# Kernel optimization log

Hardware: AMD Instinct MI355X
Metric: run time of the kernel (lower is better)

## Reference

```python
import jax, jax.numpy as jnp
import numpy as np

N = 262144      # total nodes
G = 256         # graphs
P = 1024        # nodes per graph (k=None sort pool keeps all)
E = 4194304     # edges
F_IN = 128
H = 32
C = 10          # out capsules / classes
OUT_LEN = 16
IN_LEN = 96     # 3 * 32 concat
NUM_ITERS = 3


def setup_inputs() -> dict:
    key = jax.random.key(0)
    ks = jax.random.split(key, 12)
    x = jax.random.normal(ks[0], (N, F_IN), jnp.float32)
    # edges within each graph of size P
    src = jax.random.randint(ks[1], (E,), 0, N)
    off = jax.random.randint(ks[2], (E,), 0, P)
    dst = (src // P) * P + off
    edge_index = jnp.stack([src, dst]).astype(jnp.int64)
    batch = jnp.repeat(jnp.arange(G), P).astype(jnp.int64)
    W1 = jax.random.normal(ks[3], (F_IN, H), jnp.float32) / np.sqrt(F_IN)
    b1 = jnp.zeros((H,), jnp.float32)
    W2 = jax.random.normal(ks[4], (H, H), jnp.float32) / np.sqrt(H)
    b2 = jnp.zeros((H,), jnp.float32)
    W3 = jax.random.normal(ks[5], (H, H), jnp.float32) / np.sqrt(H)
    b3 = jnp.zeros((H,), jnp.float32)
    caps_W = jax.random.normal(ks[6], (C, OUT_LEN, IN_LEN), jnp.float32) * 0.05
    return {"x": x, "edge_index": edge_index, "batch": batch,
            "W1": W1, "b1": b1, "W2": W2, "b2": b2, "W3": W3, "b3": b3,
            "caps_W": caps_W}


def _position_encoding(length, dim):
    pos = jnp.arange(length, dtype=jnp.float32)[:, None]
    i = jnp.arange(dim // 2, dtype=jnp.float32)[None, :]
    ang = pos / jnp.power(10000.0, 2.0 * i / dim)
    return jnp.stack([jnp.sin(ang), jnp.cos(ang)], axis=-1).reshape(length, dim)


def _squash(v, eps=1e-12):
    n2 = jnp.sum(v * v, axis=-1, keepdims=True)
    return (n2 / (1.0 + n2)) * v / jnp.sqrt(n2 + eps)


def reference(x, edge_index, batch, W1, b1, W2, b2, W3, b3, caps_W):
    src, dst = edge_index[0], edge_index[1]
    # remove_self_loops, then GCNConv re-adds self loops with weight 1
    mask = (src != dst).astype(x.dtype)
    deg = jax.ops.segment_sum(mask, dst, num_segments=N) + 1.0
    dis = jax.lax.rsqrt(deg)                         # deg^{-1/2}
    enorm = dis[src] * dis[dst] * mask               # [E]

    def gcn(h, W, b):
        h = h @ W                                    # [N,H]
        agg = jax.ops.segment_sum(h[src] * enorm[:, None], dst, num_segments=N)
        agg = agg + h * (dis * dis)[:, None]         # self-loop term deg^{-1}
        return jnp.tanh(agg + b)

    x1 = gcn(x, W1, b1)
    x2 = gcn(x1, W2, b2)
    x3 = gcn(x2, W3, b3)
    h = jnp.concatenate([x1, x2, x3], axis=-1)       # [N, 96]

    # global_sort_pool (k=None): per-graph sort by last channel, descending
    hg = h.reshape(G, P, IN_LEN)
    order = jnp.argsort(-hg[:, :, -1], axis=1)
    hs = jnp.take_along_axis(hg, order[:, :, None], axis=1)  # [G,P,96]
    hs = hs + _position_encoding(P, IN_LEN)[None]

    # CapsuleLinear, shared weight: priors [G, C, P, OUT_LEN]
    priors = jnp.einsum('oji,gki->gokj', caps_W, hs)

    # k-means routing
    v = jnp.mean(priors, axis=2, keepdims=True)      # [G,C,1,OUT_LEN]
    for _ in range(NUM_ITERS):
        vn = v / (jnp.linalg.norm(v, axis=-1, keepdims=True) + 1e-12)
        logits = jnp.sum(priors * vn, axis=-1, keepdims=True)  # [G,C,P,1]
        prob = jax.nn.softmax(logits, axis=2)
        v = jnp.sum(prob * priors, axis=2, keepdims=True)
    out = _squash(v)[:, :, 0, :]                     # [G, C, OUT_LEN]
    return jnp.linalg.norm(out, axis=-1)             # [G, C]
```

## Files before the change

kernel.cpp:

```cpp
#include <hip/hip_runtime.h>
#include <hip/hip_fp16.h>
#include <cstdint>
#include <cstddef>

#define N_NODES   262144
#define NG        256
#define PP        1024
#define NE        4194304
#define FIN       128
#define HH        32
#define NC        10
#define OL        16
#define IL        96
#define NITER     3
#define ECHUNK    4096
#define NCHUNK    (NE/ECHUNK)
#define ECAP      18432
#define HSTR      36

typedef _Float16 half8 __attribute__((ext_vector_type(8)));
typedef float f32x4 __attribute__((ext_vector_type(4)));

__global__ void k_hist(const int* __restrict__ ei, unsigned* __restrict__ histT) {
  __shared__ unsigned lh[NG];
  int t = threadIdx.x, b = blockIdx.x;
  lh[t] = 0;
  __syncthreads();
  int base = b * ECHUNK;
  for (int q = t; q < ECHUNK; q += 256) {
    int e = base + q;
    int s = ei[e], d = ei[NE + e];
    if (s != d) atomicAdd(&lh[s >> 10], 1u);
  }
  __syncthreads();
  histT[t * NCHUNK + b] = lh[t];
}

__global__ void k_scanA(const unsigned* __restrict__ histT, unsigned* __restrict__ cbaseT,
                        unsigned* __restrict__ gtot) {
  __shared__ unsigned wtot[4];
  int t = threadIdx.x, g = blockIdx.x;
  int lane = t & 63, wv = t >> 6;
  uint4 hv = *(const uint4*)(histT + (size_t)g * NCHUNK + t * 4);
  unsigned s0 = hv.x, s1 = s0 + hv.y, s2 = s1 + hv.z, s3 = s2 + hv.w;
  unsigned tsum = s3, sc = tsum;
  for (int d = 1; d < 64; d <<= 1) {
    unsigned v = __shfl_up(sc, d, 64);
    if (lane >= d) sc += v;
  }
  if (lane == 63) wtot[wv] = sc;
  __syncthreads();
  unsigned woff = 0;
  for (int w = 0; w < wv; ++w) woff += wtot[w];
  unsigned base = woff + sc - tsum;
  cbaseT[(size_t)(t * 4 + 0) * NG + g] = base;
  cbaseT[(size_t)(t * 4 + 1) * NG + g] = base + s0;
  cbaseT[(size_t)(t * 4 + 2) * NG + g] = base + s1;
  cbaseT[(size_t)(t * 4 + 3) * NG + g] = base + s2;
  if (t == 255) gtot[g] = woff + sc;
}

__global__ void k_scanB(const unsigned* __restrict__ gtot, unsigned* __restrict__ gbase) {
  __shared__ unsigned wtot[4];
  int t = threadIdx.x;
  int lane = t & 63, wv = t >> 6;
  unsigned x = gtot[t], sc = x;
  for (int d = 1; d < 64; d <<= 1) {
    unsigned v = __shfl_up(sc, d, 64);
    if (lane >= d) sc += v;
  }
  if (lane == 63) wtot[wv] = sc;
  __syncthreads();
  unsigned woff = 0;
  for (int w = 0; w < wv; ++w) woff += wtot[w];
  gbase[t] = woff + sc - x;
  if (t == 255) gbase[256] = woff + sc;
}

__global__ void k_scatter(const int* __restrict__ ei, const unsigned* __restrict__ cbaseT,
                          const unsigned* __restrict__ gbase, unsigned* __restrict__ epack) {
  __shared__ unsigned lcur[NG];
  int t = threadIdx.x, b = blockIdx.x;
  lcur[t] = gbase[t] + cbaseT[(size_t)b * NG + t];
  __syncthreads();
  int base = b * ECHUNK;
  for (int q = t; q < ECHUNK; q += 256) {
    int e = base + q;
    int s = ei[e], d = ei[NE + e];
    if (s != d) {
      int g = s >> 10;
      unsigned pos = atomicAdd(&lcur[g], 1u);
      epack[pos] = (unsigned)(s & 1023) | ((unsigned)(d & 1023) << 10);
    }
  }
}

__global__ __launch_bounds__(256) void k_dstsort(const unsigned* __restrict__ epack,
                          const unsigned* __restrict__ gbase,
                          unsigned short* __restrict__ esrc16,
                          unsigned* __restrict__ dstptr) {
  __shared__ unsigned shist[PP];
  __shared__ unsigned wsum[256];
  __shared__ unsigned cur[PP];
  int t = threadIdx.x, g = blockIdx.x;
  unsigned e0 = gbase[g], e1 = gbase[g + 1];
  for (int i = t; i < PP; i += 256) shist[i] = 0;
  __syncthreads();
  for (unsigned e = e0 + t; e < e1; e += 256)
    atomicAdd(&shist[(epack[e] >> 10) & 1023], 1u);
  __syncthreads();
  unsigned h0 = shist[4 * t], h1 = shist[4 * t + 1], h2 = shist[4 * t + 2], h3 = shist[4 * t + 3];
  unsigned tsum = h0 + h1 + h2 + h3;
  wsum[t] = tsum;
  __syncthreads();
  for (int off = 1; off < 256; off <<= 1) {
    unsigned v = (t >= off) ? wsum[t - off] : 0u;
    __syncthreads();
    wsum[t] += v;
    __syncthreads();
  }
  unsigned excl = wsum[t] - tsum;
  unsigned c0 = excl, c1 = c0 + h0, c2 = c1 + h1, c3 = c2 + h2;
  cur[4 * t] = c0; cur[4 * t + 1] = c1; cur[4 * t + 2] = c2; cur[4 * t + 3] = c3;
  unsigned* dp = dstptr + (size_t)g * (PP + 1);
  dp[4 * t] = c0; dp[4 * t + 1] = c1; dp[4 * t + 2] = c2; dp[4 * t + 3] = c3;
  if (t == 0) dp[PP] = e1 - e0;
  __syncthreads();
  unsigned short* eg = esrc16 + (size_t)g * ECAP;
  for (unsigned e = e0 + t; e < e1; e += 256) {
    unsigned pk = epack[e];
    unsigned so = pk & 1023, dofs = (pk >> 10) & 1023;
    unsigned pos = atomicAdd(&cur[dofs], 1u);
    if (pos < ECAP) eg[pos] = (unsigned short)so;
  }
}

__global__ void k_dis(const unsigned* __restrict__ dstptr, float* __restrict__ dis) {
  int n = blockIdx.x * 256 + threadIdx.x;
  int g = n >> 10, k = n & 1023;
  const unsigned* dp = dstptr + (size_t)g * (PP + 1) + k;
  float deg = (float)(dp[1] - dp[0]);
  dis[n] = 1.0f / sqrtf(deg + 1.0f);
}

__device__ __forceinline__ void gcn_layer(float* hsl, const float* dg, const unsigned* dp,
                                          const unsigned short* eg, const float* bias,
                                          int coloff, const float* Wn, float* hbase, int t) {
  float4 bl[8];
#pragma unroll
  for (int j = 0; j < 8; ++j) bl[j] = ((const float4*)bias)[j];
  if (Wn) {
#pragma unroll
    for (int pp = 0; pp < 8; ++pp) {
      int p = t + pp * 512;
      hsl[(p >> 2) * HSTR + 32 + (p & 3)] = Wn[p];
    }
  }
  float xn[2][32];
#pragma unroll
  for (int pth = 0; pth < 2; ++pth) {
    int k = t + pth * 512;
    float dk = dg[k];
    unsigned e0 = dp[k], e1 = dp[k + 1];
    if (e1 > (unsigned)ECAP) e1 = ECAP;
    float4 acc[8];
    const float* sp = &hsl[k * HSTR];
#pragma unroll
    for (int j = 0; j < 8; ++j) acc[j] = *(const float4*)(sp + 4 * j);
    unsigned e = e0;
    for (; e + 1 < e1; e += 2) {
      int s0 = eg[e], s1 = eg[e + 1];
      const float* q0 = &hsl[s0 * HSTR];
      const float* q1 = &hsl[s1 * HSTR];
#pragma unroll
      for (int j = 0; j < 8; ++j) {
        float4 a = *(const float4*)(q0 + 4 * j);
        float4 b2 = *(const float4*)(q1 + 4 * j);
        acc[j].x += a.x + b2.x; acc[j].y += a.y + b2.y;
        acc[j].z += a.z + b2.z; acc[j].w += a.w + b2.w;
      }
    }
    if (e < e1) {
      int s0 = eg[e];
      const float* q0 = &hsl[s0 * HSTR];
#pragma unroll
      for (int j = 0; j < 8; ++j) {
        float4 a = *(const float4*)(q0 + 4 * j);
        acc[j].x += a.x; acc[j].y += a.y; acc[j].z += a.z; acc[j].w += a.w;
      }
    }
#pragma unroll
    for (int j = 0; j < 8; ++j) {
      xn[pth][4 * j + 0] = tanhf(dk * acc[j].x + bl[j].x);
      xn[pth][4 * j + 1] = tanhf(dk * acc[j].y + bl[j].y);
      xn[pth][4 * j + 2] = tanhf(dk * acc[j].z + bl[j].z);
      xn[pth][4 * j + 3] = tanhf(dk * acc[j].w + bl[j].w);
    }
    float* hr = hbase + (size_t)k * IL + coloff;
#pragma unroll
    for (int j = 0; j < 8; ++j) {
      float4 s;
      s.x = xn[pth][4 * j]; s.y = xn[pth][4 * j + 1];
      s.z = xn[pth][4 * j + 2]; s.w = xn[pth][4 * j + 3];
      *(float4*)(hr + 4 * j) = s;
    }
  }
  __syncthreads();
  if (Wn) {
#pragma unroll
    for (int pth = 0; pth < 2; ++pth) {
      int k = t + pth * 512;
      float dk = dg[k];
      float4 o4[8];
#pragma unroll
      for (int j = 0; j < 8; ++j) { o4[j].x = 0.f; o4[j].y = 0.f; o4[j].z = 0.f; o4[j].w = 0.f; }
#pragma unroll
      for (int c = 0; c < 32; ++c) {
        float xc = xn[pth][c];
#pragma unroll
        for (int j4 = 0; j4 < 8; ++j4) {
          float4 w = *(const float4*)&hsl[(c * 8 + j4) * HSTR + 32];
          o4[j4].x += xc * w.x; o4[j4].y += xc * w.y;
          o4[j4].z += xc * w.z; o4[j4].w += xc * w.w;
        }
      }
      float* op = &hsl[k * HSTR];
#pragma unroll
      for (int j4 = 0; j4 < 8; ++j4) {
        float4 s;
        s.x = o4[j4].x * dk; s.y = o4[j4].y * dk;
        s.z = o4[j4].z * dk; s.w = o4[j4].w * dk;
        *(float4*)(op + 4 * j4) = s;
      }
    }
    __syncthreads();
  }
}

__global__ __launch_bounds__(512) void k_gcn(const float* __restrict__ x,
                                             const float* __restrict__ dis,
                                             const unsigned short* __restrict__ esrc16,
                                             const unsigned* __restrict__ dstptr,
                                             const float* __restrict__ W1, const float* __restrict__ b1,
                                             const float* __restrict__ W2, const float* __restrict__ b2,
                                             const float* __restrict__ W3, const float* __restrict__ b3,
                                             float* __restrict__ h) {
  __shared__ float hsl[PP * HSTR];
  int t = threadIdx.x, g = blockIdx.x;
  const float* dg = dis + (size_t)g * PP;
  const unsigned* dp = dstptr + (size_t)g * (PP + 1);
  const unsigned short* eg = esrc16 + (size_t)g * ECAP;
  float* hbase = h + (size_t)g * PP * IL;

#pragma unroll
  for (int pp = 0; pp < 8; ++pp) {
    int p = t + pp * 512;
    hsl[(p >> 2) * HSTR + 32 + (p & 3)] = W1[p];
  }
  __syncthreads();

  {
    int cg = t & 3, ng = t >> 2;
    int row0 = ng * 8;
    const float* xr = x + ((size_t)g * PP + row0) * FIN;
    float acc[8][8];
#pragma unroll
    for (int r = 0; r < 8; ++r)
#pragma unroll
      for (int j = 0; j < 8; ++j) acc[r][j] = 0.f;
    for (int k4 = 0; k4 < FIN / 4; ++k4) {
      float4 xv[8];
#pragma unroll
      for (int r = 0; r < 8; ++r)
        xv[r] = *(const float4*)(xr + (size_t)r * FIN + k4 * 4);
#pragma unroll
      for (int kk = 0; kk < 4; ++kk) {
        int k = k4 * 4 + kk;
        float4 wa = *(const float4*)&hsl[(k * 8 + cg * 2) * HSTR + 32];
        float4 wb = *(const float4*)&hsl[(k * 8 + cg * 2 + 1) * HSTR + 32];
#pragma unroll
        for (int r = 0; r < 8; ++r) {
          float xk = kk == 0 ? xv[r].x : kk == 1 ? xv[r].y : kk == 2 ? xv[r].z : xv[r].w;
          acc[r][0] += xk * wa.x; acc[r][1] += xk * wa.y;
          acc[r][2] += xk * wa.z; acc[r][3] += xk * wa.w;
          acc[r][4] += xk * wb.x; acc[r][5] += xk * wb.y;
          acc[r][6] += xk * wb.z; acc[r][7] += xk * wb.w;
        }
      }
    }
#pragma unroll
    for (int r = 0; r < 8; ++r) {
      float d = dg[row0 + r];
      float4 s0, s1;
      s0.x = acc[r][0] * d; s0.y = acc[r][1] * d; s0.z = acc[r][2] * d; s0.w = acc[r][3] * d;
      s1.x = acc[r][4] * d; s1.y = acc[r][5] * d; s1.z = acc[r][6] * d; s1.w = acc[r][7] * d;
      *(float4*)&hsl[(row0 + r) * HSTR + cg * 8] = s0;
      *(float4*)&hsl[(row0 + r) * HSTR + cg * 8 + 4] = s1;
    }
  }
  __syncthreads();

  gcn_layer(hsl, dg, dp, eg, b1, 0,  W2, hbase, t);
  gcn_layer(hsl, dg, dp, eg, b2, 32, W3, hbase, t);
  gcn_layer(hsl, dg, dp, eg, b3, 64, nullptr, hbase, t);
}

__global__ __launch_bounds__(512) void k_sort(const float* __restrict__ h,
                                              unsigned short* __restrict__ rank16) {
  __shared__ float key[PP];
  __shared__ unsigned sidx[PP];
  int t = threadIdx.x, g = blockIdx.x;
  for (int i = t; i < PP; i += 512) {
    key[i] = h[(size_t)(g * PP + i) * IL + (IL - 1)];
    sidx[i] = i;
  }
  __syncthreads();
  for (int sz = 2; sz <= PP; sz <<= 1) {
    for (int st = sz >> 1; st > 0; st >>= 1) {
      int i = 2 * t - (t & (st - 1));
      int j = i + st;
      float ki = key[i], kj = key[j];
      unsigned ii = sidx[i], ij = sidx[j];
      bool less_ji = (kj > ki) || (kj == ki && ij < ii);
      bool asc = ((i & sz) == 0);
      if (less_ji == asc) { key[i] = kj; key[j] = ki; sidx[i] = ij; sidx[j] = ii; }
      __syncthreads();
    }
  }
  for (int i = t; i < PP; i += 512) rank16[g * PP + sidx[i]] = (unsigned short)i;
}

__global__ void k_pe(float* __restrict__ pe) {
  int id = blockIdx.x * 256 + threadIdx.x;
  if (id >= PP * 48) return;
  int pos = id / 48, i = id % 48;
  float denom = powf(10000.0f, (2.0f * i) / 96.0f);
  float ang = (float)pos / denom;
  pe[pos * IL + 2 * i] = sinf(ang);
  pe[pos * IL + 2 * i + 1] = cosf(ang);
}

__global__ void k_wpe(const float* __restrict__ pe, const float* __restrict__ capsW,
                      __half* __restrict__ wpe) {
  int id = blockIdx.x * 256 + threadIdx.x;
  if (id >= NC * PP * OL) return;
  int j = id & 15;
  int pos = (id >> 4) & 1023;
  int c = id >> 14;
  const float* wr = capsW + (size_t)(c * OL + j) * IL;
  const float* pr = pe + (size_t)pos * IL;
  float a = 0;
#pragma unroll 8
  for (int i = 0; i < IL; ++i) a += wr[i] * pr[i];
  wpe[(((size_t)c << 10) + pos) * 16 + j] = __float2half(a);
}

__global__ __launch_bounds__(256) void k_pgemm(const float* __restrict__ h,
                                               const float* __restrict__ capsW,
                                               __half* __restrict__ Pc) {
  int t = threadIdx.x, b = blockIdx.x;
  int g = b >> 2;
  int wv = t >> 6, lane = t & 63;
  int quad = lane >> 4, l16 = lane & 15;
  half8 afr[4][3];
#pragma unroll
  for (int rt = 0; rt < 4; ++rt) {
    int row = b * 256 + wv * 64 + rt * 16 + l16;
    const float* hr = h + (size_t)row * IL + quad * 8;
#pragma unroll
    for (int kb = 0; kb < 3; ++kb) {
      float4 x = *(const float4*)(hr + kb * 32);
      float4 y = *(const float4*)(hr + kb * 32 + 4);
      half8 a;
      a[0] = (_Float16)x.x; a[1] = (_Float16)x.y; a[2] = (_Float16)x.z; a[3] = (_Float16)x.w;
      a[4] = (_Float16)y.x; a[5] = (_Float16)y.y; a[6] = (_Float16)y.z; a[7] = (_Float16)y.w;
      afr[rt][kb] = a;
    }
  }
  int krow_base = (b & 3) * 256 + wv * 64;
  for (int ct = 0; ct < NC; ++ct) {
    half8 bfr[3];
    const float* wr = capsW + (size_t)(ct * 16 + l16) * IL + quad * 8;
#pragma unroll
    for (int kb = 0; kb < 3; ++kb) {
      float4 x = *(const float4*)(wr + kb * 32);
      float4 y = *(const float4*)(wr + kb * 32 + 4);
      half8 bb;
      bb[0] = (_Float16)x.x; bb[1] = (_Float16)x.y; bb[2] = (_Float16)x.z; bb[3] = (_Float16)x.w;
      bb[4] = (_Float16)y.x; bb[5] = (_Float16)y.y; bb[6] = (_Float16)y.z; bb[7] = (_Float16)y.w;
      bfr[kb] = bb;
    }
#pragma unroll
    for (int rt = 0; rt < 4; ++rt) {
      f32x4 acc = {0.f, 0.f, 0.f, 0.f};
      acc = __builtin_amdgcn_mfma_f32_16x16x32_f16(afr[rt][0], bfr[0], acc, 0, 0, 0);
      acc = __builtin_amdgcn_mfma_f32_16x16x32_f16(afr[rt][1], bfr[1], acc, 0, 0, 0);
      acc = __builtin_amdgcn_mfma_f32_16x16x32_f16(afr[rt][2], bfr[2], acc, 0, 0, 0);
      int krow = krow_base + rt * 16;
      __half* po = Pc + ((((size_t)g * NC + ct) << 10) + krow) * 16 + l16;
#pragma unroll
      for (int r = 0; r < 4; ++r)
        po[(quad * 4 + r) * 16] = __float2half(acc[r]);
    }
  }
}

__global__ __launch_bounds__(256) void k_route2(const __half* __restrict__ Pc,
                                                const __half* __restrict__ wpe,
                                                const unsigned short* __restrict__ rank16,
                                                float* __restrict__ out) {
  __shared__ float v_l[16];
  __shared__ float wred[4][17];
  int t = threadIdx.x;
  int gc = blockIdx.x;
  int g = gc / NC, c = gc - g * NC;
  int lane = t & 63, wv = t >> 6;
  const __half* pg = Pc + ((size_t)gc << 10) * 16;
  const unsigned short* rk = rank16 + (size_t)g * PP;
  const __half* wc = wpe + ((size_t)c << 10) * 16;
  float pr[4][16];
  float vsum[16];
#pragma unroll
  for (int i = 0; i < 16; ++i) vsum[i] = 0.f;
#pragma unroll
  for (int r = 0; r < 4; ++r) {
    int k = t + r * 256;
    uint4 a0 = *(const uint4*)(pg + (size_t)k * 16);
    uint4 a1 = *(const uint4*)(pg + (size_t)k * 16 + 8);
    int rkk = rk[k];
    uint4 b0 = *(const uint4*)(wc + (size_t)rkk * 16);
    uint4 b1 = *(const uint4*)(wc + (size_t)rkk * 16 + 8);
    const __half2* pa0 = (const __half2*)&a0; const __half2* pa1 = (const __half2*)&a1;
    const __half2* pb0 = (const __half2*)&b0; const __half2* pb1 = (const __half2*)&b1;
#pragma unroll
    for (int j = 0; j < 4; ++j) {
      float2 fa = __half22float2(pa0[j]); float2 fb = __half22float2(pb0[j]);
      pr[r][2 * j] = fa.x + fb.x; pr[r][2 * j + 1] = fa.y + fb.y;
      float2 fa1 = __half22float2(pa1[j]); float2 fb1 = __half22float2(pb1[j]);
      pr[r][8 + 2 * j] = fa1.x + fb1.x; pr[r][8 + 2 * j + 1] = fa1.y + fb1.y;
    }
#pragma unroll
    for (int i = 0; i < 16; ++i) vsum[i] += pr[r][i];
  }
#pragma unroll
  for (int d = 1; d < 64; d <<= 1)
#pragma unroll
    for (int i = 0; i < 16; ++i) vsum[i] += __shfl_xor(vsum[i], d, 64);
  if (lane == 0) {
#pragma unroll
    for (int i = 0; i < 16; ++i) wred[wv][i] = vsum[i];
  }
  __syncthreads();
  if (t < 16) v_l[t] = wred[0][t] + wred[1][t] + wred[2][t] + wred[3][t];
  __syncthreads();
  for (int it = 0; it < NITER; ++it) {
    float vn[16]; float n2 = 0;
#pragma unroll
    for (int i = 0; i < 16; ++i) { float x = v_l[i]; vn[i] = x; n2 += x * x; }
    float inv = 1.0f / (sqrtf(n2) + 1e-12f);
#pragma unroll
    for (int i = 0; i < 16; ++i) vn[i] *= inv;
    float lg[4];
#pragma unroll
    for (int r = 0; r < 4; ++r) {
      float a = 0;
#pragma unroll
      for (int i = 0; i < 16; ++i) a += pr[r][i] * vn[i];
      lg[r] = a;
    }
    float mx = fmaxf(fmaxf(lg[0], lg[1]), fmaxf(lg[2], lg[3]));
#pragma unroll
    for (int d = 1; d < 64; d <<= 1) mx = fmaxf(mx, __shfl_xor(mx, d, 64));
    __syncthreads();
    if (lane == 0) wred[wv][16] = mx;
    __syncthreads();
    float gmax = fmaxf(fmaxf(wred[0][16], wred[1][16]), fmaxf(wred[2][16], wred[3][16]));
    float es = 0; float eacc[16];
#pragma unroll
    for (int i = 0; i < 16; ++i) eacc[i] = 0.f;
#pragma unroll
    for (int r = 0; r < 4; ++r) {
      float e = __expf(lg[r] - gmax);
      es += e;
#pragma unroll
      for (int i = 0; i < 16; ++i) eacc[i] += e * pr[r][i];
    }
#pragma unroll
    for (int d = 1; d < 64; d <<= 1) {
      es += __shfl_xor(es, d, 64);
#pragma unroll
      for (int i = 0; i < 16; ++i) eacc[i] += __shfl_xor(eacc[i], d, 64);
    }
    __syncthreads();
    if (lane == 0) {
#pragma unroll
      for (int i = 0; i < 16; ++i) wred[wv][i] = eacc[i];
      wred[wv][16] = es;
    }
    __syncthreads();
    if (t < 16) {
      float s = wred[0][t] + wred[1][t] + wred[2][t] + wred[3][t];
      float S = wred[0][16] + wred[1][16] + wred[2][16] + wred[3][16];
      v_l[t] = s / S;
    }
    __syncthreads();
  }
  if (t == 0) {
    float n2 = 0;
#pragma unroll
    for (int i = 0; i < 16; ++i) { float x = v_l[i]; n2 += x * x; }
    out[gc] = (n2 / (1.0f + n2)) * sqrtf(n2) / sqrtf(n2 + 1e-12f);
  }
}

extern "C" void kernel_launch(void* const* d_in, const int* in_sizes, int n_in,
                              void* d_out, int out_size, void* d_ws, size_t ws_size,
                              hipStream_t stream) {
  const float* x     = (const float*)d_in[0];
  const int*   ei    = (const int*)d_in[1];
  const float* W1    = (const float*)d_in[3];
  const float* b1    = (const float*)d_in[4];
  const float* W2    = (const float*)d_in[5];
  const float* b2    = (const float*)d_in[6];
  const float* W3    = (const float*)d_in[7];
  const float* b3    = (const float*)d_in[8];
  const float* capsW = (const float*)d_in[9];
  float* out = (float*)d_out;

  char* wp = (char*)d_ws;
  auto alloc = [&](size_t bytes) { char* p = wp; wp += (bytes + 255) & ~(size_t)255; return p; };
  float*    dis    = (float*)alloc((size_t)N_NODES * 4);
  float*    h      = (float*)alloc((size_t)N_NODES * IL * 4);
  char*     ureg   = wp;
  unsigned* epack  = (unsigned*)alloc((size_t)NE * 4);
  unsigned short* esrc16 = (unsigned short*)alloc((size_t)NG * ECAP * 2);
  unsigned* histT  = (unsigned*)alloc((size_t)NCHUNK * NG * 4);
  unsigned* cbaseT = (unsigned*)alloc((size_t)NCHUNK * NG * 4);
  const size_t PC_BYTES = (size_t)NG * NC * PP * 16 * 2;
  if ((size_t)(wp - ureg) < PC_BYTES) wp = ureg + ((PC_BYTES + 255) & ~(size_t)255);
  __half*   Pc     = (__half*)ureg;
  unsigned* gtot   = (unsigned*)alloc((size_t)NG * 4);
  unsigned* gbase  = (unsigned*)alloc((size_t)(NG + 1) * 4);
  unsigned* dstptr = (unsigned*)alloc((size_t)NG * (PP + 1) * 4);
  unsigned short* rank16 = (unsigned short*)alloc((size_t)NG * PP * 2);
  float*    pe     = (float*)alloc((size_t)PP * IL * 4);
  __half*   wpe    = (__half*)alloc((size_t)NC * PP * OL * 2);

  k_hist<<<NCHUNK, 256, 0, stream>>>(ei, histT);
  k_scanA<<<NG, 256, 0, stream>>>(histT, cbaseT, gtot);
  k_scanB<<<1, 256, 0, stream>>>(gtot, gbase);
  k_scatter<<<NCHUNK, 256, 0, stream>>>(ei, cbaseT, gbase, epack);
  k_dstsort<<<NG, 256, 0, stream>>>(epack, gbase, esrc16, dstptr);
  k_dis<<<N_NODES / 256, 256, 0, stream>>>(dstptr, dis);
  k_pe<<<(PP * 48) / 256, 256, 0, stream>>>(pe);
  k_wpe<<<(NC * PP * OL) / 256, 256, 0, stream>>>(pe, capsW, wpe);

  k_gcn<<<NG, 512, 0, stream>>>(x, dis, esrc16, dstptr, W1, b1, W2, b2, W3, b3, h);

  k_sort<<<NG, 512, 0, stream>>>(h, rank16);
  k_pgemm<<<N_NODES / 256, 256, 0, stream>>>(h, capsW, Pc);
  k_route2<<<NG * NC, 256, 0, stream>>>(Pc, wpe, rank16, out);
}
```

Baseline: 628.6 us.

## Convert GCN features to fp16 storage, MFMA first layer, swizzled LDS, fast tanh

The fused GCN kernel now keeps node features in shared memory as fp16 with an XOR-swizzled layout, accumulates neighbours with packed half2 adds, and computes the first projection x@W1 with MFMA f16 instead of scalar FMAs. Concatenated activations go to global memory as fp16, which halves the write and the later read in the capsule GEMM, and the sort key is written to its own small array. tanh is replaced with an exp-based approximation, and W2/W3 are read straight from global memory instead of being staged in LDS. The fp16 accumulation over many neighbours risks precision loss and overflow, and the smaller LDS footprint allows more blocks per CU.

```diff
diff --git a/kernel.cpp b/kernel.cpp
--- a/kernel.cpp
+++ b/kernel.cpp
@@ -16,10 +16,28 @@
 #define ECHUNK    4096
 #define NCHUNK    (NE/ECHUNK)
 #define ECAP      18432
-#define HSTR      36
 
 typedef _Float16 half8 __attribute__((ext_vector_type(8)));
 typedef float f32x4 __attribute__((ext_vector_type(4)));
+
+__device__ __forceinline__ float tanh_fast(float x) {
+  float e = __expf(2.0f * x);
+  return 1.0f - 2.0f / (e + 1.0f);
+}
+__device__ __forceinline__ unsigned pk2(float a, float b) {
+  __half2 h = __floats2half2_rn(a, b);
+  union { __half2 h; unsigned u; } v; v.h = h; return v.u;
+}
+__device__ __forceinline__ __half2 u2h2(unsigned u) {
+  union { unsigned u; __half2 h; } v; v.u = u; return v.h;
+}
+
+__device__ __forceinline__ int hslc(int row, int c) {
+  return row * 32 + ((c ^ ((row >> 1) & 3)) << 3);
+}
+__device__ __forceinline__ int hslh(int row, int halfcol) {
+  return hslc(row, halfcol >> 3) + (halfcol & 7);
+}
 
 __global__ void k_hist(const int* __restrict__ ei, unsigned* __restrict__ histT) {
   __shared__ unsigned lh[NG];
@@ -143,67 +161,92 @@
   dis[n] = 1.0f / sqrtf(deg + 1.0f);
 }
 
-__device__ __forceinline__ void gcn_layer(float* hsl, const float* dg, const unsigned* dp,
+__device__ __forceinline__ void gcn_layer(__half* hsl, const float* dg, const unsigned* dp,
                                           const unsigned short* eg, const float* bias,
-                                          int coloff, const float* Wn, float* hbase, int t) {
-  float4 bl[8];
-#pragma unroll
-  for (int j = 0; j < 8; ++j) bl[j] = ((const float4*)bias)[j];
-  if (Wn) {
-#pragma unroll
-    for (int pp = 0; pp < 8; ++pp) {
-      int p = t + pp * 512;
-      hsl[(p >> 2) * HSTR + 32 + (p & 3)] = Wn[p];
-    }
-  }
-  float xn[2][32];
+                                          int coloff, const float* Wn, __half* hb16,
+                                          float* keyArr, int t) {
+  unsigned xnu[2][16];
 #pragma unroll
   for (int pth = 0; pth < 2; ++pth) {
     int k = t + pth * 512;
     float dk = dg[k];
     unsigned e0 = dp[k], e1 = dp[k + 1];
     if (e1 > (unsigned)ECAP) e1 = ECAP;
-    float4 acc[8];
-    const float* sp = &hsl[k * HSTR];
-#pragma unroll
-    for (int j = 0; j < 8; ++j) acc[j] = *(const float4*)(sp + 4 * j);
+    __half2 acc2[16];
+    {
+      uint4 u0 = *(const uint4*)&hsl[hslc(k, 0)];
+      uint4 u1 = *(const uint4*)&hsl[hslc(k, 1)];
+      uint4 u2 = *(const uint4*)&hsl[hslc(k, 2)];
+      uint4 u3 = *(const uint4*)&hsl[hslc(k, 3)];
+      acc2[0] = u2h2(u0.x); acc2[1] = u2h2(u0.y); acc2[2] = u2h2(u0.z); acc2[3] = u2h2(u0.w);
+      acc2[4] = u2h2(u1.x); acc2[5] = u2h2(u1.y); acc2[6] = u2h2(u1.z); acc2[7] = u2h2(u1.w);
+      acc2[8] = u2h2(u2.x); acc2[9] = u2h2(u2.y); acc2[10] = u2h2(u2.z); acc2[11] = u2h2(u2.w);
+      acc2[12] = u2h2(u3.x); acc2[13] = u2h2(u3.y); acc2[14] = u2h2(u3.z); acc2[15] = u2h2(u3.w);
+    }
     unsigned e = e0;
     for (; e + 1 < e1; e += 2) {
       int s0 = eg[e], s1 = eg[e + 1];
-      const float* q0 = &hsl[s0 * HSTR];
-      const float* q1 = &hsl[s1 * HSTR];
-#pragma unroll
-      for (int j = 0; j < 8; ++j) {
-        float4 a = *(const float4*)(q0 + 4 * j);
-        float4 b2 = *(const float4*)(q1 + 4 * j);
-        acc[j].x += a.x + b2.x; acc[j].y += a.y + b2.y;
-        acc[j].z += a.z + b2.z; acc[j].w += a.w + b2.w;
-      }
+      uint4 a0 = *(const uint4*)&hsl[hslc(s0, 0)];
+      uint4 a1 = *(const uint4*)&hsl[hslc(s0, 1)];
+      uint4 a2 = *(const uint4*)&hsl[hslc(s0, 2)];
+      uint4 a3 = *(const uint4*)&hsl[hslc(s0, 3)];
+      uint4 b0 = *(const uint4*)&hsl[hslc(s1, 0)];
+      uint4 b1 = *(const uint4*)&hsl[hslc(s1, 1)];
+      uint4 b2 = *(const uint4*)&hsl[hslc(s1, 2)];
+      uint4 b3 = *(const uint4*)&hsl[hslc(s1, 3)];
+      acc2[0] = __hadd2(acc2[0], __hadd2(u2h2(a0.x), u2h2(b0.x)));
+      acc2[1] = __hadd2(acc2[1], __hadd2(u2h2(a0.y), u2h2(b0.y)));
+      acc2[2] = __hadd2(acc2[2], __hadd2(u2h2(a0.z), u2h2(b0.z)));
+      acc2[3] = __hadd2(acc2[3], __hadd2(u2h2(a0.w), u2h2(b0.w)));
+      acc2[4] = __hadd2(acc2[4], __hadd2(u2h2(a1.x), u2h2(b1.x)));
+      acc2[5] = __hadd2(acc2[5], __hadd2(u2h2(a1.y), u2h2(b1.y)));
+      acc2[6] = __hadd2(acc2[6], __hadd2(u2h2(a1.z), u2h2(b1.z)));
+      acc2[7] = __hadd2(acc2[7], __hadd2(u2h2(a1.w), u2h2(b1.w)));
+      acc2[8] = __hadd2(acc2[8], __hadd2(u2h2(a2.x), u2h2(b2.x)));
+      acc2[9] = __hadd2(acc2[9], __hadd2(u2h2(a2.y), u2h2(b2.y)));
+      acc2[10] = __hadd2(acc2[10], __hadd2(u2h2(a2.z), u2h2(b2.z)));
+      acc2[11] = __hadd2(acc2[11], __hadd2(u2h2(a2.w), u2h2(b2.w)));
+      acc2[12] = __hadd2(acc2[12], __hadd2(u2h2(a3.x), u2h2(b3.x)));
+      acc2[13] = __hadd2(acc2[13], __hadd2(u2h2(a3.y), u2h2(b3.y)));
+      acc2[14] = __hadd2(acc2[14], __hadd2(u2h2(a3.z), u2h2(b3.z)));
+      acc2[15] = __hadd2(acc2[15], __hadd2(u2h2(a3.w), u2h2(b3.w)));
     }
     if (e < e1) {
       int s0 = eg[e];
-      const float* q0 = &hsl[s0 * HSTR];
-#pragma unroll
-      for (int j = 0; j < 8; ++j) {
-        float4 a = *(const float4*)(q0 + 4 * j);
-        acc[j].x += a.x; acc[j].y += a.y; acc[j].z += a.z; acc[j].w += a.w;
-      }
-    }
-#pragma unroll
-    for (int j = 0; j < 8; ++j) {
-      xn[pth][4 * j + 0] = tanhf(dk * acc[j].x + bl[j].x);
-      xn[pth][4 * j + 1] = tanhf(dk * acc[j].y + bl[j].y);
-      xn[pth][4 * j + 2] = tanhf(dk * acc[j].z + bl[j].z);
-      xn[pth][4 * j + 3] = tanhf(dk * acc[j].w + bl[j].w);
-    }
-    float* hr = hbase + (size_t)k * IL + coloff;
-#pragma unroll
-    for (int j = 0; j < 8; ++j) {
-      float4 s;
-      s.x = xn[pth][4 * j]; s.y = xn[pth][4 * j + 1];
-      s.z = xn[pth][4 * j + 2]; s.w = xn[pth][4 * j + 3];
-      *(float4*)(hr + 4 * j) = s;
-    }
+      uint4 a0 = *(const uint4*)&hsl[hslc(s0, 0)];
+      uint4 a1 = *(const uint4*)&hsl[hslc(s0, 1)];
+      uint4 a2 = *(const uint4*)&hsl[hslc(s0, 2)];
+      uint4 a3 = *(const uint4*)&hsl[hslc(s0, 3)];
+      acc2[0] = __hadd2(acc2[0], u2h2(a0.x)); acc2[1] = __hadd2(acc2[1], u2h2(a0.y));
+      acc2[2] = __hadd2(acc2[2], u2h2(a0.z)); acc2[3] = __hadd2(acc2[3], u2h2(a0.w));
+      acc2[4] = __hadd2(acc2[4], u2h2(a1.x)); acc2[5] = __hadd2(acc2[5], u2h2(a1.y));
+      acc2[6] = __hadd2(acc2[6], u2h2(a1.z)); acc2[7] = __hadd2(acc2[7], u2h2(a1.w));
+      acc2[8] = __hadd2(acc2[8], u2h2(a2.x)); acc2[9] = __hadd2(acc2[9], u2h2(a2.y));
+      acc2[10] = __hadd2(acc2[10], u2h2(a2.z)); acc2[11] = __hadd2(acc2[11], u2h2(a2.w));
+      acc2[12] = __hadd2(acc2[12], u2h2(a3.x)); acc2[13] = __hadd2(acc2[13], u2h2(a3.y));
+      acc2[14] = __hadd2(acc2[14], u2h2(a3.z)); acc2[15] = __hadd2(acc2[15], u2h2(a3.w));
+    }
+    float lastv = 0.f;
+#pragma unroll
+    for (int i = 0; i < 16; ++i) {
+      float2 f = __half22float2(acc2[i]);
+      float a0 = tanh_fast(dk * f.x + bias[2 * i]);
+      float a1 = tanh_fast(dk * f.y + bias[2 * i + 1]);
+      xnu[pth][i] = pk2(a0, a1);
+      if (i == 15) lastv = a1;
+    }
+    __half* hr = hb16 + (size_t)k * IL + coloff;
+    uint4 h0, h1;
+    h0.x = xnu[pth][0]; h0.y = xnu[pth][1]; h0.z = xnu[pth][2]; h0.w = xnu[pth][3];
+    h1.x = xnu[pth][4]; h1.y = xnu[pth][5]; h1.z = xnu[pth][6]; h1.w = xnu[pth][7];
+    ((uint4*)hr)[0] = h0;
+    ((uint4*)hr)[1] = h1;
+    uint4 h2, h3;
+    h2.x = xnu[pth][8]; h2.y = xnu[pth][9]; h2.z = xnu[pth][10]; h2.w = xnu[pth][11];
+    h3.x = xnu[pth][12]; h3.y = xnu[pth][13]; h3.z = xnu[pth][14]; h3.w = xnu[pth][15];
+    ((uint4*)hr)[2] = h2;
+    ((uint4*)hr)[3] = h3;
+    if (keyArr) keyArr[k] = lastv;
   }
   __syncthreads();
   if (Wn) {
@@ -215,103 +258,107 @@
 #pragma unroll
       for (int j = 0; j < 8; ++j) { o4[j].x = 0.f; o4[j].y = 0.f; o4[j].z = 0.f; o4[j].w = 0.f; }
 #pragma unroll
-      for (int c = 0; c < 32; ++c) {
-        float xc = xn[pth][c];
+      for (int c2 = 0; c2 < 16; ++c2) {
+        float2 xc = __half22float2(u2h2(xnu[pth][c2]));
+        const float4* wr0 = (const float4*)(Wn + (2 * c2) * 32);
+        const float4* wr1 = (const float4*)(Wn + (2 * c2 + 1) * 32);
 #pragma unroll
         for (int j4 = 0; j4 < 8; ++j4) {
-          float4 w = *(const float4*)&hsl[(c * 8 + j4) * HSTR + 32];
-          o4[j4].x += xc * w.x; o4[j4].y += xc * w.y;
-          o4[j4].z += xc * w.z; o4[j4].w += xc * w.w;
+          float4 w0 = wr0[j4], w1 = wr1[j4];
+          o4[j4].x += xc.x * w0.x + xc.y * w1.x;
+          o4[j4].y += xc.x * w0.y + xc.y * w1.y;
+          o4[j4].z += xc.x * w0.z + xc.y * w1.z;
+          o4[j4].w += xc.x * w0.w + xc.y * w1.w;
         }
       }
-      float* op = &hsl[k * HSTR];
-#pragma unroll
-      for (int j4 = 0; j4 < 8; ++j4) {
-        float4 s;
-        s.x = o4[j4].x * dk; s.y = o4[j4].y * dk;
-        s.z = o4[j4].z * dk; s.w = o4[j4].w * dk;
-        *(float4*)(op + 4 * j4) = s;
+#pragma unroll
+      for (int c = 0; c < 4; ++c) {
+        uint4 u;
+        u.x = pk2(o4[2 * c].x * dk, o4[2 * c].y * dk);
+        u.y = pk2(o4[2 * c].z * dk, o4[2 * c].w * dk);
+        u.z = pk2(o4[2 * c + 1].x * dk, o4[2 * c + 1].y * dk);
+        u.w = pk2(o4[2 * c + 1].z * dk, o4[2 * c + 1].w * dk);
+        *(uint4*)&hsl[hslc(k, c)] = u;
       }
     }
     __syncthreads();
   }
 }
 
-__global__ __launch_bounds__(512) void k_gcn(const float* __restrict__ x,
+__global__ __launch_bounds__(512, 4) void k_gcn(const float* __restrict__ x,
                                              const float* __restrict__ dis,
                                              const unsigned short* __restrict__ esrc16,
                                              const unsigned* __restrict__ dstptr,
                                              const float* __restrict__ W1, const float* __restrict__ b1,
                                              const float* __restrict__ W2, const float* __restrict__ b2,
                                              const float* __restrict__ W3, const float* __restrict__ b3,
-                                             float* __restrict__ h) {
-  __shared__ float hsl[PP * HSTR];
+                                             __half* __restrict__ h16, float* __restrict__ key) {
+  __shared__ __half hsl[PP * 32];
   int t = threadIdx.x, g = blockIdx.x;
   const float* dg = dis + (size_t)g * PP;
   const unsigned* dp = dstptr + (size_t)g * (PP + 1);
   const unsigned short* eg = esrc16 + (size_t)g * ECAP;
-  float* hbase = h + (size_t)g * PP * IL;
-
-#pragma unroll
-  for (int pp = 0; pp < 8; ++pp) {
-    int p = t + pp * 512;
-    hsl[(p >> 2) * HSTR + 32 + (p & 3)] = W1[p];
-  }
-  __syncthreads();
+  __half* hb16 = h16 + (size_t)g * PP * IL;
+  float* keyg = key + (size_t)g * PP;
 
   {
-    int cg = t & 3, ng = t >> 2;
-    int row0 = ng * 8;
-    const float* xr = x + ((size_t)g * PP + row0) * FIN;
-    float acc[8][8];
-#pragma unroll
-    for (int r = 0; r < 8; ++r)
-#pragma unroll
-      for (int j = 0; j < 8; ++j) acc[r][j] = 0.f;
-    for (int k4 = 0; k4 < FIN / 4; ++k4) {
-      float4 xv[8];
-#pragma unroll
-      for (int r = 0; r < 8; ++r)
-        xv[r] = *(const float4*)(xr + (size_t)r * FIN + k4 * 4);
-#pragma unroll
-      for (int kk = 0; kk < 4; ++kk) {
-        int k = k4 * 4 + kk;
-        float4 wa = *(const float4*)&hsl[(k * 8 + cg * 2) * HSTR + 32];
-        float4 wb = *(const float4*)&hsl[(k * 8 + cg * 2 + 1) * HSTR + 32];
-#pragma unroll
-        for (int r = 0; r < 8; ++r) {
-          float xk = kk == 0 ? xv[r].x : kk == 1 ? xv[r].y : kk == 2 ? xv[r].z : xv[r].w;
-          acc[r][0] += xk * wa.x; acc[r][1] += xk * wa.y;
-          acc[r][2] += xk * wa.z; acc[r][3] += xk * wa.w;
-          acc[r][4] += xk * wb.x; acc[r][5] += xk * wb.y;
-          acc[r][6] += xk * wb.z; acc[r][7] += xk * wb.w;
-        }
+    int wv = t >> 6, lane = t & 63, quad = lane >> 4, l16 = lane & 15;
+    half8 bfr[2][4];
+#pragma unroll
+    for (int nt = 0; nt < 2; ++nt)
+#pragma unroll
+      for (int kf = 0; kf < 4; ++kf) {
+        half8 bb;
+#pragma unroll
+        for (int j = 0; j < 8; ++j)
+          bb[j] = (_Float16)W1[(kf * 32 + quad * 8 + j) * HH + nt * 16 + l16];
+        bfr[nt][kf] = bb;
       }
-    }
-#pragma unroll
-    for (int r = 0; r < 8; ++r) {
-      float d = dg[row0 + r];
-      float4 s0, s1;
-      s0.x = acc[r][0] * d; s0.y = acc[r][1] * d; s0.z = acc[r][2] * d; s0.w = acc[r][3] * d;
-      s1.x = acc[r][4] * d; s1.y = acc[r][5] * d; s1.z = acc[r][6] * d; s1.w = acc[r][7] * d;
-      *(float4*)&hsl[(row0 + r) * HSTR + cg * 8] = s0;
-      *(float4*)&hsl[(row0 + r) * HSTR + cg * 8 + 4] = s1;
-    }
-  }
-  __syncthreads();
-
-  gcn_layer(hsl, dg, dp, eg, b1, 0,  W2, hbase, t);
-  gcn_layer(hsl, dg, dp, eg, b2, 32, W3, hbase, t);
-  gcn_layer(hsl, dg, dp, eg, b3, 64, nullptr, hbase, t);
-}
-
-__global__ __launch_bounds__(512) void k_sort(const float* __restrict__ h,
+#pragma unroll
+    for (int rt = 0; rt < 8; ++rt) {
+      int row = wv * 128 + rt * 16 + l16;
+      const float* xr = x + ((size_t)g * PP + row) * FIN;
+      half8 af[4];
+#pragma unroll
+      for (int kf = 0; kf < 4; ++kf) {
+        float4 xa = *(const float4*)(xr + kf * 32 + quad * 8);
+        float4 xb = *(const float4*)(xr + kf * 32 + quad * 8 + 4);
+        half8 a;
+        a[0] = (_Float16)xa.x; a[1] = (_Float16)xa.y; a[2] = (_Float16)xa.z; a[3] = (_Float16)xa.w;
+        a[4] = (_Float16)xb.x; a[5] = (_Float16)xb.y; a[6] = (_Float16)xb.z; a[7] = (_Float16)xb.w;
+        af[kf] = a;
+      }
+      int rb = wv * 128 + rt * 16 + quad * 4;
+      float dv0 = dg[rb], dv1 = dg[rb + 1], dv2 = dg[rb + 2], dv3 = dg[rb + 3];
+#pragma unroll
+      for (int nt = 0; nt < 2; ++nt) {
+        f32x4 acc = {0.f, 0.f, 0.f, 0.f};
+        acc = __builtin_amdgcn_mfma_f32_16x16x32_f16(af[0], bfr[nt][0], acc, 0, 0, 0);
+        acc = __builtin_amdgcn_mfma_f32_16x16x32_f16(af[1], bfr[nt][1], acc, 0, 0, 0);
+        acc = __builtin_amdgcn_mfma_f32_16x16x32_f16(af[2], bfr[nt][2], acc, 0, 0, 0);
+        acc = __builtin_amdgcn_mfma_f32_16x16x32_f16(af[3], bfr[nt][3], acc, 0, 0, 0);
+        int col = nt * 16 + l16;
+        hsl[hslh(rb + 0, col)] = __float2half(acc[0] * dv0);
+        hsl[hslh(rb + 1, col)] = __float2half(acc[1] * dv1);
+        hsl[hslh(rb + 2, col)] = __float2half(acc[2] * dv2);
+        hsl[hslh(rb + 3, col)] = __float2half(acc[3] * dv3);
+      }
+    }
+  }
+  __syncthreads();
+
+  gcn_layer(hsl, dg, dp, eg, b1, 0,  W2, hb16, nullptr, t);
+  gcn_layer(hsl, dg, dp, eg, b2, 32, W3, hb16, nullptr, t);
+  gcn_layer(hsl, dg, dp, eg, b3, 64, nullptr, hb16, keyg, t);
+}
+
+__global__ __launch_bounds__(512) void k_sort(const float* __restrict__ keyArr,
                                               unsigned short* __restrict__ rank16) {
   __shared__ float key[PP];
   __shared__ unsigned sidx[PP];
   int t = threadIdx.x, g = blockIdx.x;
   for (int i = t; i < PP; i += 512) {
-    key[i] = h[(size_t)(g * PP + i) * IL + (IL - 1)];
+    key[i] = keyArr[(size_t)g * PP + i];
     sidx[i] = i;
   }
   __syncthreads();
@@ -355,7 +402,7 @@
   wpe[(((size_t)c << 10) + pos) * 16 + j] = __float2half(a);
 }
 
-__global__ __launch_bounds__(256) void k_pgemm(const float* __restrict__ h,
+__global__ __launch_bounds__(256) void k_pgemm(const __half* __restrict__ h16,
                                                const float* __restrict__ capsW,
                                                __half* __restrict__ Pc) {
   int t = threadIdx.x, b = blockIdx.x;
@@ -366,15 +413,11 @@
 #pragma unroll
   for (int rt = 0; rt < 4; ++rt) {
     int row = b * 256 + wv * 64 + rt * 16 + l16;
-    const float* hr = h + (size_t)row * IL + quad * 8;
+    const __half* hr = h16 + (size_t)row * IL + quad * 8;
 #pragma unroll
     for (int kb = 0; kb < 3; ++kb) {
-      float4 x = *(const float4*)(hr + kb * 32);
-      float4 y = *(const float4*)(hr + kb * 32 + 4);
-      half8 a;
-      a[0] = (_Float16)x.x; a[1] = (_Float16)x.y; a[2] = (_Float16)x.z; a[3] = (_Float16)x.w;
-      a[4] = (_Float16)y.x; a[5] = (_Float16)y.y; a[6] = (_Float16)y.z; a[7] = (_Float16)y.w;
-      afr[rt][kb] = a;
+      uint4 u = *(const uint4*)(hr + kb * 32);
+      afr[rt][kb] = __builtin_bit_cast(half8, u);
     }
   }
   int krow_base = (b & 3) * 256 + wv * 64;
@@ -383,11 +426,11 @@
     const float* wr = capsW + (size_t)(ct * 16 + l16) * IL + quad * 8;
 #pragma unroll
     for (int kb = 0; kb < 3; ++kb) {
-      float4 x = *(const float4*)(wr + kb * 32);
-      float4 y = *(const float4*)(wr + kb * 32 + 4);
+      float4 xx = *(const float4*)(wr + kb * 32);
+      float4 yy = *(const float4*)(wr + kb * 32 + 4);
       half8 bb;
-      bb[0] = (_Float16)x.x; bb[1] = (_Float16)x.y; bb[2] = (_Float16)x.z; bb[3] = (_Float16)x.w;
-      bb[4] = (_Float16)y.x; bb[5] = (_Float16)y.y; bb[6] = (_Float16)y.z; bb[7] = (_Float16)y.w;
+      bb[0] = (_Float16)xx.x; bb[1] = (_Float16)xx.y; bb[2] = (_Float16)xx.z; bb[3] = (_Float16)xx.w;
+      bb[4] = (_Float16)yy.x; bb[5] = (_Float16)yy.y; bb[6] = (_Float16)yy.z; bb[7] = (_Float16)yy.w;
       bfr[kb] = bb;
     }
 #pragma unroll
@@ -530,7 +573,8 @@
   char* wp = (char*)d_ws;
   auto alloc = [&](size_t bytes) { char* p = wp; wp += (bytes + 255) & ~(size_t)255; return p; };
   float*    dis    = (float*)alloc((size_t)N_NODES * 4);
-  float*    h      = (float*)alloc((size_t)N_NODES * IL * 4);
+  __half*   h16    = (__half*)alloc((size_t)N_NODES * IL * 2);
+  float*    key    = (float*)alloc((size_t)N_NODES * 4);
   char*     ureg   = wp;
   unsigned* epack  = (unsigned*)alloc((size_t)NE * 4);
   unsigned short* esrc16 = (unsigned short*)alloc((size_t)NG * ECAP * 2);
@@ -555,9 +599,9 @@
   k_pe<<<(PP * 48) / 256, 256, 0, stream>>>(pe);
   k_wpe<<<(NC * PP * OL) / 256, 256, 0, stream>>>(pe, capsW, wpe);
 
-  k_gcn<<<NG, 512, 0, stream>>>(x, dis, esrc16, dstptr, W1, b1, W2, b2, W3, b3, h);
-
-  k_sort<<<NG, 512, 0, stream>>>(h, rank16);
-  k_pgemm<<<N_NODES / 256, 256, 0, stream>>>(h, capsW, Pc);
+  k_gcn<<<NG, 512, 0, stream>>>(x, dis, esrc16, dstptr, W1, b1, W2, b2, W3, b3, h16, key);
+
+  k_sort<<<NG, 512, 0, stream>>>(key, rank16);
+  k_pgemm<<<N_NODES / 256, 256, 0, stream>>>(h16, capsW, Pc);
   k_route2<<<NG * NC, 256, 0, stream>>>(Pc, wpe, rank16, out);
 }
```

After: 654.2 us. 4.1% more time.
